# Kernel tuning notes

Measured on AMD Instinct MI355X. Metric: run time of the kernel, lower is better.

Reference implementation:

```python
import jax, jax.numpy as jnp
import numpy as np
import math

B, T, D, H = 2, 2048, 1024, 16
DH = D // H  # 64


def _rope_tables(seq_len, dim, dtype=jnp.float32):
    inv_freq = 1.0 / (10000.0 ** (jnp.arange(0, dim, 2, dtype=jnp.float32) / dim))
    t = jnp.arange(seq_len, dtype=jnp.float32)
    freqs = jnp.outer(t, inv_freq)  # [T, dim/2]
    return jnp.cos(freqs).astype(dtype), jnp.sin(freqs).astype(dtype)


def apply_rotary(x, cos, sin):
    # x: [B,H,T,DH]; cos/sin: [1,1,T,DH/2]
    d = x.shape[-1]
    x1, x2 = x[..., : d // 2], x[..., d // 2 :]
    return jnp.concatenate([x1 * cos - x2 * sin, x2 * cos + x1 * sin], axis=-1)


def setup_inputs() -> dict:
    key = jax.random.key(0)
    k1, k2, k3 = jax.random.split(key, 3)
    x = jax.random.normal(k1, (B, T, D), dtype=jnp.float32)
    Wqkv = jax.random.normal(k2, (D, 3 * D), dtype=jnp.float32) * (1.0 / math.sqrt(D))
    Wout = jax.random.normal(k3, (D, D), dtype=jnp.float32) * (1.0 / math.sqrt(D))
    cos, sin = _rope_tables(T, DH)  # [T, 32]
    mask = jnp.tril(jnp.ones((T, T), dtype=bool))[None, None]  # causal [1,1,T,T]
    return {"x": x, "Wqkv": Wqkv, "Wout": Wout, "cos": cos, "sin": sin, "mask": mask}


def reference(x, Wqkv, Wout, cos, sin, mask):
    Bb, Tt, C = x.shape
    qkv = (x @ Wqkv).reshape(Bb, Tt, 3, H, DH)
    q = jnp.transpose(qkv[:, :, 0], (0, 2, 1, 3))  # [B,H,T,DH]
    k = jnp.transpose(qkv[:, :, 1], (0, 2, 1, 3))
    v = jnp.transpose(qkv[:, :, 2], (0, 2, 1, 3))
    c = cos[None, None]  # [1,1,T,DH/2]
    s = sin[None, None]
    q = apply_rotary(q, c, s)
    k = apply_rotary(k, c, s)
    attn = jnp.einsum("bhqd,bhkd->bhqk", q, k) / math.sqrt(DH)
    attn = jnp.where(mask, attn, jnp.float32(-jnp.inf))
    attn = jax.nn.softmax(attn, axis=-1)  # dropout p=0 (eval)
    out = jnp.einsum("bhqk,bhkd->bhqd", attn, v)
    out = jnp.transpose(out, (0, 2, 1, 3)).reshape(Bb, Tt, C)
    return out @ Wout
```

## Files before the change

### kernel.cpp

```cpp
#include <hip/hip_runtime.h>
#include <hip/hip_bf16.h>

#define B_ 2
#define T_ 2048
#define D_ 1024
#define H_ 16
#define DH_ 64
#define N3_ 3072
#define M_ 4096

typedef __attribute__((ext_vector_type(8))) short short8;
typedef __attribute__((ext_vector_type(4))) float f32x4;
typedef __attribute__((ext_vector_type(4))) unsigned short ushort4v;

__device__ __forceinline__ unsigned short f2bf(float f) {
  return __builtin_bit_cast(unsigned short, __hip_bfloat16(f));
}
__device__ __forceinline__ float bf2f(unsigned short u) {
  union { unsigned u; float f; } v; v.u = ((unsigned)u) << 16;
  return v.f;
}

__device__ __forceinline__ void gload_lds16(const unsigned short* g, unsigned short* l) {
  __builtin_amdgcn_global_load_lds((const __attribute__((address_space(1))) void*)g,
                                   (__attribute__((address_space(3))) void*)l, 16, 0, 0);
}

__global__ __launch_bounds__(256)
void k_prep(const float* __restrict__ x, const float* __restrict__ Wqkv,
            const float* __restrict__ Wout, unsigned short* __restrict__ Xb,
            unsigned short* __restrict__ Wqkv_t, unsigned short* __restrict__ Wout_t) {
  __shared__ float tile[64][65];
  const int bid = blockIdx.x;
  if (bid < 4096) {
    int i = (bid * 256 + threadIdx.x) * 4;
    f32x4 v = *(const f32x4*)&x[i];
    ushort4v o;
    o[0] = f2bf(v[0]); o[1] = f2bf(v[1]); o[2] = f2bf(v[2]); o[3] = f2bf(v[3]);
    *(ushort4v*)&Xb[i] = o;
    return;
  }
  const float* in;
  unsigned short* out;
  int R, C, bx, by;
  if (bid < 4096 + 768) {
    int t = bid - 4096; in = Wqkv; out = Wqkv_t; R = 1024; C = 3072;
    bx = t % 48; by = t / 48;
  } else {
    int t = bid - 4864; in = Wout; out = Wout_t; R = 1024; C = 1024;
    bx = t & 15; by = t >> 4;
  }
  int c0 = bx * 64, r0 = by * 64;
  int tx = threadIdx.x & 63, ty = threadIdx.x >> 6;
#pragma unroll
  for (int i = 0; i < 64; i += 4)
    tile[ty + i][tx] = in[(size_t)(r0 + ty + i) * C + c0 + tx];
  __syncthreads();
#pragma unroll
  for (int i = 0; i < 64; i += 4)
    out[(size_t)(c0 + ty + i) * R + r0 + tx] = f2bf(tile[tx][ty + i]);
}

#define GEMM_DBUF_LOOP(A_, Bt_, Kx_)                                               \
  const int l4 = lane >> 2, c4 = lane & 3;                                         \
  const int srcswz = ((c4 ^ (l4 & 3) ^ ((l4 >> 2) & 3)) << 3);                     \
  const int fswz = (((l15 & 3) ^ ((l15 >> 2) & 3)) << 3);                          \
  auto stage = [&](int buf, int k0) {                                              \
    _Pragma("unroll")                                                              \
    for (int i = 0; i < 2; ++i)                                                    \
      gload_lds16(&A_[(size_t)(m0 + wid * 32 + i * 16 + l4) * Kx_ + k0 + srcswz],  \
                  &As[buf * 4096 + (wid * 32 + i * 16) * 32]);                     \
    _Pragma("unroll")                                                              \
    for (int i = 0; i < 2; ++i)                                                    \
      gload_lds16(&Bt_[(size_t)(n0 + wid * 32 + i * 16 + l4) * Kx_ + k0 + srcswz], \
                  &Bs[buf * 4096 + (wid * 32 + i * 16) * 32]);                     \
  };                                                                               \
  const int KI = (Kx_) >> 5;                                                       \
  stage(0, 0);                                                                     \
  for (int it = 0; it < KI; ++it) {                                                \
    __syncthreads();                                                               \
    if (it + 1 < KI) stage((it + 1) & 1, (it + 1) << 5);                           \
    const unsigned short* As_ = &As[(it & 1) * 4096];                              \
    const unsigned short* Bs_ = &Bs[(it & 1) * 4096];                              \
    short8 af[4], bfr[4];                                                          \
    _Pragma("unroll")                                                              \
    for (int mi = 0; mi < 4; ++mi)                                                 \
      af[mi] = *(const short8*)&As_[(wr * 64 + mi * 16 + l15) * 32 +               \
                                    ((lg << 3) ^ fswz)];                           \
    _Pragma("unroll")                                                              \
    for (int ni = 0; ni < 4; ++ni)                                                 \
      bfr[ni] = *(const short8*)&Bs_[(wc * 64 + ni * 16 + l15) * 32 +              \
                                     ((lg << 3) ^ fswz)];                          \
    _Pragma("unroll")                                                              \
    for (int mi = 0; mi < 4; ++mi)                                                 \
      _Pragma("unroll")                                                            \
      for (int ni = 0; ni < 4; ++ni)                                               \
        acc[mi][ni] = __builtin_amdgcn_mfma_f32_16x16x32_bf16(af[mi], bfr[ni],     \
                                                              acc[mi][ni], 0, 0, 0); \
  }

template <typename OUT_T>
__global__ __launch_bounds__(256)
void k_gemm_bt(const unsigned short* __restrict__ A, const unsigned short* __restrict__ Bt,
               OUT_T* __restrict__ C, int Mx, int Nx, int Kx) {
  __shared__ __align__(16) unsigned short As[2 * 128 * 32];
  __shared__ __align__(16) unsigned short Bs[2 * 128 * 32];
  const int tid = threadIdx.x;
  const int lane = tid & 63;
  const int l15 = lane & 15, lg = lane >> 4;
  const int wid = tid >> 6;
  const int wr = wid >> 1, wc = wid & 1;
  const int m0 = blockIdx.y * 128, n0 = blockIdx.x * 128;

  const f32x4 zero4 = {0.f, 0.f, 0.f, 0.f};
  f32x4 acc[4][4];
#pragma unroll
  for (int mi = 0; mi < 4; ++mi)
#pragma unroll
    for (int ni = 0; ni < 4; ++ni) acc[mi][ni] = zero4;

  GEMM_DBUF_LOOP(A, Bt, Kx)

#pragma unroll
  for (int mi = 0; mi < 4; ++mi)
#pragma unroll
    for (int ni = 0; ni < 4; ++ni)
#pragma unroll
      for (int j = 0; j < 4; ++j) {
        int row = m0 + wr * 64 + mi * 16 + lg * 4 + j;
        int col = n0 + wc * 64 + ni * 16 + l15;
        float v = acc[mi][ni][j];
        if constexpr (sizeof(OUT_T) == 2) C[(size_t)row * Nx + col] = f2bf(v);
        else                              C[(size_t)row * Nx + col] = v;
      }
}

__global__ __launch_bounds__(256)
void k_gemm_qkv_rope(const unsigned short* __restrict__ A, const unsigned short* __restrict__ Bt,
                     const float* __restrict__ cosT, const float* __restrict__ sinT,
                     unsigned short* __restrict__ Q, unsigned short* __restrict__ K,
                     unsigned short* __restrict__ Vt) {
  __shared__ __align__(16) unsigned short As[2 * 128 * 32];
  __shared__ __align__(16) unsigned short Bs[2 * 128 * 32];
  const int tid = threadIdx.x;
  const int lane = tid & 63;
  const int l15 = lane & 15, lg = lane >> 4;
  const int wid = tid >> 6;
  const int wr = wid >> 1, wc = wid & 1;
  const int m0 = blockIdx.y * 128, n0 = blockIdx.x * 128;

  const f32x4 zero4 = {0.f, 0.f, 0.f, 0.f};
  f32x4 acc[4][4];
#pragma unroll
  for (int mi = 0; mi < 4; ++mi)
#pragma unroll
    for (int ni = 0; ni < 4; ++ni) acc[mi][ni] = zero4;

  GEMM_DBUF_LOOP(A, Bt, D_)

  const int region = n0 >> 10;
  const int h = (((n0 & 1023)) + wc * 64) >> 6;
  if (region < 2) {
    unsigned short* out = (region == 0) ? Q : K;
    const float scale = (region == 0) ? 0.125f : 1.f;
#pragma unroll
    for (int mi = 0; mi < 4; ++mi)
#pragma unroll
      for (int j = 0; j < 4; ++j) {
        int row = m0 + wr * 64 + mi * 16 + lg * 4 + j;
        int b = row >> 11, t = row & (T_ - 1);
        size_t obase = ((size_t)(b * H_ + h) * T_ + t) * DH_;
#pragma unroll
        for (int ni = 0; ni < 2; ++ni) {
          int dh = ni * 16 + l15;
          float cs = cosT[t * 32 + dh], sn = sinT[t * 32 + dh];
          float x1 = acc[mi][ni][j], x2 = acc[mi][ni + 2][j];
          out[obase + dh]      = f2bf((x1 * cs - x2 * sn) * scale);
          out[obase + dh + 32] = f2bf((x2 * cs + x1 * sn) * scale);
        }
      }
  } else {
#pragma unroll
    for (int mi = 0; mi < 4; ++mi) {
      int row0 = m0 + wr * 64 + mi * 16 + lg * 4;
      int b = row0 >> 11, t0 = row0 & (T_ - 1);
#pragma unroll
      for (int ni = 0; ni < 4; ++ni) {
        int col = (n0 - 2048) + wc * 64 + ni * 16 + l15;
        int hv = col >> 6, dh = col & 63;
        ushort4v pk;
#pragma unroll
        for (int j = 0; j < 4; ++j) pk[j] = f2bf(acc[mi][ni][j]);
        *(ushort4v*)&Vt[((size_t)(b * H_ + hv) * DH_ + dh) * T_ + t0] = pk;
      }
    }
  }
}

__global__ __launch_bounds__(256)
void k_attn(const unsigned short* __restrict__ Q, const unsigned short* __restrict__ K,
            const unsigned short* __restrict__ Vt, unsigned short* __restrict__ O) {
  __shared__ __align__(16) unsigned short Ks[2 * 64 * 64];
  __shared__ __align__(16) unsigned short Vs[3 * 64 * 64];
  __shared__ __align__(16) unsigned short Pl[4][16][72];
  const int tid = threadIdx.x;
  const int wid = tid >> 6, lane = tid & 63;
  const int l15 = lane & 15, lg = lane >> 4;
  const int l8 = lane >> 3, c8 = lane & 7;
  const int srcoff = (c8 ^ l8) << 3;
  const int wg = (blockIdx.x & 7) * 128 + (blockIdx.x >> 3);
  const int qb = 31 - (wg & 31);
  const int hb = wg >> 5;
  const int qblk = qb * 64;
  const int q0 = qblk + wid * 16;
  const size_t hbase = (size_t)hb * T_ * DH_;
  const unsigned short* Qh = Q + hbase;
  const unsigned short* Kh = K + hbase;
  const unsigned short* Vh = Vt + hbase;
  unsigned short* Pw = &Pl[wid][0][0];

  short8 bq0 = *(const short8*)&Qh[(q0 + l15) * DH_ + lg * 8];
  short8 bq1 = *(const short8*)&Qh[(q0 + l15) * DH_ + 32 + lg * 8];

  int koffA[4], koffB[4], voff[2][4];
#pragma unroll
  for (int g = 0; g < 4; ++g) {
    int r = g * 16 + l15;
    koffA[g] = r * 64 + (((lg)     ^ (r & 7)) << 3);
    koffB[g] = r * 64 + (((4 + lg) ^ (r & 7)) << 3);
  }
#pragma unroll
  for (int ks = 0; ks < 2; ++ks)
#pragma unroll
    for (int nb = 0; nb < 4; ++nb) {
      int r = nb * 16 + l15;
      voff[ks][nb] = r * 64 + (((ks * 4 + lg) ^ (r & 7)) << 3);
    }

  const f32x4 zero4 = {0.f, 0.f, 0.f, 0.f};
  f32x4 accO[4];
#pragma unroll
  for (int nb = 0; nb < 4; ++nb) accO[nb] = zero4;
  float m_run = -INFINITY, l_run = 0.f;
  const int qg = q0 + l15;
  const int nt = qb + 1;

  auto stage = [&](int t) {
    const int kt = t << 6;
    if (wid < 2) {
      unsigned short* kb = &Ks[(t & 1) * 4096];
      const unsigned short* Kt = Kh + (size_t)kt * DH_;
#pragma unroll
      for (int i = 0; i < 4; ++i)
        gload_lds16(&Kt[(wid * 32 + i * 8 + l8) * DH_ + srcoff],
                    &kb[(wid * 4 + i) * 512]);
    } else {
      unsigned short* vb = &Vs[(t % 3) * 4096];
      const unsigned short* Vg = Vh + kt;
#pragma unroll
      for (int i = 0; i < 4; ++i)
        gload_lds16(&Vg[((wid - 2) * 32 + i * 8 + l8) * T_ + srcoff],
                    &vb[((wid - 2) * 4 + i) * 512]);
    }
  };

  auto QKT = [&](int t, f32x4* cg) {
    const unsigned short* Kb_ = &Ks[(t & 1) * 4096];
    __builtin_amdgcn_s_setprio(1);
#pragma unroll
    for (int g = 0; g < 4; ++g) {
      short8 a0 = *(const short8*)&Kb_[koffA[g]];
      short8 a1 = *(const short8*)&Kb_[koffB[g]];
      cg[g] = __builtin_amdgcn_mfma_f32_16x16x32_bf16(a0, bq0, zero4, 0, 0, 0);
      cg[g] = __builtin_amdgcn_mfma_f32_16x16x32_bf16(a1, bq1, cg[g], 0, 0, 0);
    }
    __builtin_amdgcn_s_setprio(0);
  };

  auto SOFTPV = [&](int t, f32x4* cg) {
    const int kt = t << 6;
    const unsigned short* Vb_ = &Vs[(t % 3) * 4096];
    float s[16];
#pragma unroll
    for (int g = 0; g < 4; ++g)
#pragma unroll
      for (int j = 0; j < 4; ++j) s[g * 4 + j] = cg[g][j];
    if (kt + 63 > q0) {
#pragma unroll
      for (int g = 0; g < 4; ++g) {
        int kb0 = kt + g * 16 + lg * 4;
#pragma unroll
        for (int j = 0; j < 4; ++j)
          if (kb0 + j > qg) s[g * 4 + j] = -INFINITY;
      }
    }
    float t8[8];
#pragma unroll
    for (int j = 0; j < 8; ++j) t8[j] = fmaxf(s[j], s[j + 8]);
    float t4a = fmaxf(t8[0], t8[4]), t4b = fmaxf(t8[1], t8[5]);
    float t4c = fmaxf(t8[2], t8[6]), t4d = fmaxf(t8[3], t8[7]);
    float pm = fmaxf(fmaxf(t4a, t4b), fmaxf(t4c, t4d));
    pm = fmaxf(pm, __shfl_xor(pm, 16));
    pm = fmaxf(pm, __shfl_xor(pm, 32));
    if (!__all(pm <= m_run + 8.f)) {
      float m_new = fmaxf(m_run, pm);
      float alpha = __expf(m_run - m_new);
      float aj[4];
#pragma unroll
      for (int j = 0; j < 4; ++j) aj[j] = __shfl(alpha, lg * 4 + j);
#pragma unroll
      for (int nb = 0; nb < 4; ++nb)
#pragma unroll
        for (int j = 0; j < 4; ++j) accO[nb][j] *= aj[j];
      l_run *= alpha;
      m_run = m_new;
    }
    float p[16];
#pragma unroll
    for (int j = 0; j < 16; ++j) p[j] = __expf(s[j] - m_run);
    float u8[8];
#pragma unroll
    for (int j = 0; j < 8; ++j) u8[j] = p[j] + p[j + 8];
    float u4a = u8[0] + u8[4], u4b = u8[1] + u8[5];
    float u4c = u8[2] + u8[6], u4d = u8[3] + u8[7];
    float psum = (u4a + u4b) + (u4c + u4d);
    psum += __shfl_xor(psum, 16);
    psum += __shfl_xor(psum, 32);
    l_run += psum;
#pragma unroll
    for (int g = 0; g < 4; ++g) {
      ushort4v pk;
#pragma unroll
      for (int j = 0; j < 4; ++j) pk[j] = f2bf(p[g * 4 + j]);
      *(ushort4v*)&Pw[l15 * 72 + g * 16 + lg * 4] = pk;
    }
    __builtin_amdgcn_s_setprio(1);
#pragma unroll
    for (int ks = 0; ks < 2; ++ks) {
      short8 pa = *(const short8*)&Pw[l15 * 72 + ks * 32 + lg * 8];
#pragma unroll
      for (int nb = 0; nb < 4; ++nb) {
        short8 vb = *(const short8*)&Vb_[voff[ks][nb]];
        accO[nb] = __builtin_amdgcn_mfma_f32_16x16x32_bf16(pa, vb, accO[nb], 0, 0, 0);
      }
    }
    __builtin_amdgcn_s_setprio(0);
  };

  f32x4 cgA[4], cgB[4];
  stage(0);
  for (int t = 0; t < nt; t += 2) {
    __syncthreads();
    if (t + 1 < nt) stage(t + 1);
    QKT(t, cgA);
    if (t > 0) SOFTPV(t - 1, cgB);
    __syncthreads();
    if (t + 2 < nt) stage(t + 2);
    if (t + 1 < nt) QKT(t + 1, cgB);
    SOFTPV(t, cgA);
  }
  if ((nt & 1) == 0) SOFTPV(nt - 1, cgB);

  float lj[4];
#pragma unroll
  for (int j = 0; j < 4; ++j) lj[j] = 1.f / __shfl(l_run, lg * 4 + j);
  int b = hb >> 4, h = hb & 15;
#pragma unroll
  for (int nb = 0; nb < 4; ++nb)
#pragma unroll
    for (int j = 0; j < 4; ++j) {
      int t = q0 + lg * 4 + j;
      O[(size_t)(b * T_ + t) * D_ + h * DH_ + nb * 16 + l15] = f2bf(accO[nb][j] * lj[j]);
    }
}

extern "C" void kernel_launch(void* const* d_in, const int* in_sizes, int n_in,
                              void* d_out, int out_size, void* d_ws, size_t ws_size,
                              hipStream_t stream) {
  const float* x    = (const float*)d_in[0];
  const float* Wqkv = (const float*)d_in[1];
  const float* Wout = (const float*)d_in[2];
  const float* cosT = (const float*)d_in[3];
  const float* sinT = (const float*)d_in[4];
  float* out = (float*)d_out;
  char* ws = (char*)d_ws;
  unsigned short* Xb     = (unsigned short*)(ws);
  unsigned short* Wqkv_t = (unsigned short*)(ws + 8388608);
  unsigned short* Wout_t = (unsigned short*)(ws + 14680064);
  unsigned short* Ob     = (unsigned short*)(ws + 16777216);
  unsigned short* Qb     = (unsigned short*)(ws + 41943040);
  unsigned short* Kb     = (unsigned short*)(ws + 50331648);
  unsigned short* Vt     = (unsigned short*)(ws + 58720256);

  k_prep<<<5120, 256, 0, stream>>>(x, Wqkv, Wout, Xb, Wqkv_t, Wout_t);
  k_gemm_qkv_rope<<<dim3(24, 32), 256, 0, stream>>>(Xb, Wqkv_t, cosT, sinT, Qb, Kb, Vt);
  k_attn<<<1024, 256, 0, stream>>>(Qb, Kb, Vt, Ob);
  k_gemm_bt<float><<<dim3(8, 32), 256, 0, stream>>>(Ob, Wout_t, out, 4096, 1024, 1024);
}
```

Before: 131.2 us.

## Enlarge QKV GEMM tile to 256x256 with 512 threads and K-step 64

Restructures the fused QKV projection plus RoPE kernel from 128x128 tiles with 4 waves to 256x256 tiles with 8 waves, each wave computing a 128x64 sub-tile. It uses an inline double-buffered pipeline with K-step 64 and XOR-swizzled LDS. The aim is more operand reuse per global load and fewer K-loop barriers. In exchange, the grid drops to 192 blocks, fewer than the CU count. LDS use rises to 128KB per block, which likely allows only one block per CU.

```diff
diff --git a/kernel.cpp b/kernel.cpp
--- a/kernel.cpp
+++ b/kernel.cpp
@@ -135,54 +135,102 @@
       }
 }
 
-__global__ __launch_bounds__(256)
+__global__ __launch_bounds__(512, 2)
 void k_gemm_qkv_rope(const unsigned short* __restrict__ A, const unsigned short* __restrict__ Bt,
                      const float* __restrict__ cosT, const float* __restrict__ sinT,
                      unsigned short* __restrict__ Q, unsigned short* __restrict__ K,
                      unsigned short* __restrict__ Vt) {
-  __shared__ __align__(16) unsigned short As[2 * 128 * 32];
-  __shared__ __align__(16) unsigned short Bs[2 * 128 * 32];
+  __shared__ __align__(16) unsigned short As[2 * 256 * 64];
+  __shared__ __align__(16) unsigned short Bs[2 * 256 * 64];
+  const int Kx = D_;
   const int tid = threadIdx.x;
   const int lane = tid & 63;
   const int l15 = lane & 15, lg = lane >> 4;
+  const int l8 = lane >> 3, c8 = lane & 7;
+  const int srcoff = (c8 ^ l8) << 3;
   const int wid = tid >> 6;
-  const int wr = wid >> 1, wc = wid & 1;
-  const int m0 = blockIdx.y * 128, n0 = blockIdx.x * 128;
+  const int wr = wid >> 2, wc = wid & 3;
+  const int m0 = blockIdx.y * 256, n0 = blockIdx.x * 256;
 
   const f32x4 zero4 = {0.f, 0.f, 0.f, 0.f};
-  f32x4 acc[4][4];
-#pragma unroll
-  for (int mi = 0; mi < 4; ++mi)
-#pragma unroll
-    for (int ni = 0; ni < 4; ++ni) acc[mi][ni] = zero4;
-
-  GEMM_DBUF_LOOP(A, Bt, D_)
+  f32x4 acc[8][4];
+#pragma unroll
+  for (int ar = 0; ar < 8; ++ar)
+#pragma unroll
+    for (int ni = 0; ni < 4; ++ni) acc[ar][ni] = zero4;
+
+  auto stage = [&](int t) {
+    const int k0 = t << 6;
+    unsigned short* abuf = &As[(t & 1) * 16384];
+    unsigned short* bbuf = &Bs[(t & 1) * 16384];
+#pragma unroll
+    for (int i = 0; i < 4; ++i)
+      gload_lds16(&A[(size_t)(m0 + wid * 32 + i * 8 + l8) * Kx + k0 + srcoff],
+                  &abuf[(wid * 32 + i * 8) * 64]);
+#pragma unroll
+    for (int i = 0; i < 4; ++i)
+      gload_lds16(&Bt[(size_t)(n0 + wid * 32 + i * 8 + l8) * Kx + k0 + srcoff],
+                  &bbuf[(wid * 32 + i * 8) * 64]);
+  };
+
+  stage(0);
+  asm volatile("s_waitcnt vmcnt(0)\ns_barrier" ::: "memory");
+  for (int t = 0; t < 16; ++t) {
+    if (t + 1 < 16) stage(t + 1);
+    const unsigned short* As_ = &As[(t & 1) * 16384];
+    const unsigned short* Bs_ = &Bs[(t & 1) * 16384];
+#pragma unroll
+    for (int kk = 0; kk < 2; ++kk) {
+      short8 bf[4];
+#pragma unroll
+      for (int ni = 0; ni < 4; ++ni) {
+        int r = wc * 64 + ni * 16 + l15;
+        bf[ni] = *(const short8*)&Bs_[r * 64 + (((kk * 4 + lg) ^ (r & 7)) << 3)];
+      }
+#pragma unroll
+      for (int mh = 0; mh < 2; ++mh) {
+        short8 af[4];
+#pragma unroll
+        for (int mi = 0; mi < 4; ++mi) {
+          int r = wr * 128 + mh * 64 + mi * 16 + l15;
+          af[mi] = *(const short8*)&As_[r * 64 + (((kk * 4 + lg) ^ (r & 7)) << 3)];
+        }
+#pragma unroll
+        for (int mi = 0; mi < 4; ++mi)
+#pragma unroll
+          for (int ni = 0; ni < 4; ++ni)
+            acc[mh * 4 + mi][ni] = __builtin_amdgcn_mfma_f32_16x16x32_bf16(
+                af[mi], bf[ni], acc[mh * 4 + mi][ni], 0, 0, 0);
+      }
+    }
+    asm volatile("s_waitcnt vmcnt(0)\ns_barrier" ::: "memory");
+  }
 
   const int region = n0 >> 10;
-  const int h = (((n0 & 1023)) + wc * 64) >> 6;
+  const int h = ((n0 & 1023) + wc * 64) >> 6;
   if (region < 2) {
     unsigned short* out = (region == 0) ? Q : K;
     const float scale = (region == 0) ? 0.125f : 1.f;
 #pragma unroll
-    for (int mi = 0; mi < 4; ++mi)
+    for (int ar = 0; ar < 8; ++ar)
 #pragma unroll
       for (int j = 0; j < 4; ++j) {
-        int row = m0 + wr * 64 + mi * 16 + lg * 4 + j;
-        int b = row >> 11, t = row & (T_ - 1);
-        size_t obase = ((size_t)(b * H_ + h) * T_ + t) * DH_;
+        int row = m0 + wr * 128 + ar * 16 + lg * 4 + j;
+        int b = row >> 11, tt = row & (T_ - 1);
+        size_t obase = ((size_t)(b * H_ + h) * T_ + tt) * DH_;
 #pragma unroll
         for (int ni = 0; ni < 2; ++ni) {
           int dh = ni * 16 + l15;
-          float cs = cosT[t * 32 + dh], sn = sinT[t * 32 + dh];
-          float x1 = acc[mi][ni][j], x2 = acc[mi][ni + 2][j];
+          float cs = cosT[tt * 32 + dh], sn = sinT[tt * 32 + dh];
+          float x1 = acc[ar][ni][j], x2 = acc[ar][ni + 2][j];
           out[obase + dh]      = f2bf((x1 * cs - x2 * sn) * scale);
           out[obase + dh + 32] = f2bf((x2 * cs + x1 * sn) * scale);
         }
       }
   } else {
 #pragma unroll
-    for (int mi = 0; mi < 4; ++mi) {
-      int row0 = m0 + wr * 64 + mi * 16 + lg * 4;
+    for (int ar = 0; ar < 8; ++ar) {
+      int row0 = m0 + wr * 128 + ar * 16 + lg * 4;
       int b = row0 >> 11, t0 = row0 & (T_ - 1);
 #pragma unroll
       for (int ni = 0; ni < 4; ++ni) {
@@ -190,7 +238,7 @@
         int hv = col >> 6, dh = col & 63;
         ushort4v pk;
 #pragma unroll
-        for (int j = 0; j < 4; ++j) pk[j] = f2bf(acc[mi][ni][j]);
+        for (int j = 0; j < 4; ++j) pk[j] = f2bf(acc[ar][ni][j]);
         *(ushort4v*)&Vt[((size_t)(b * H_ + hv) * DH_ + dh) * T_ + t0] = pk;
       }
     }
@@ -393,7 +441,7 @@
   unsigned short* Vt     = (unsigned short*)(ws + 58720256);
 
   k_prep<<<5120, 256, 0, stream>>>(x, Wqkv, Wout, Xb, Wqkv_t, Wout_t);
-  k_gemm_qkv_rope<<<dim3(24, 32), 256, 0, stream>>>(Xb, Wqkv_t, cosT, sinT, Qb, Kb, Vt);
+  k_gemm_qkv_rope<<<dim3(12, 16), 512, 0, stream>>>(Xb, Wqkv_t, cosT, sinT, Qb, Kb, Vt);
   k_attn<<<1024, 256, 0, stream>>>(Qb, Kb, Vt, Ob);
   k_gemm_bt<float><<<dim3(8, 32), 256, 0, stream>>>(Ob, Wout_t, out, 4096, 1024, 1024);
 }
```

Result: no change. 130.4 us (-0.6%).
